# Performance work log

Hardware: AMD Instinct MI355X
Metric: run time of the kernel (lower is better)

## Reference

```python
import jax, jax.numpy as jnp
import numpy as np

B, N, D = 32, 64, 64  # batch, num_points, hidden_dim


def _dense_init(key, fan_in, fan_out):
    kw, kb = jax.random.split(key)
    W = jax.random.normal(kw, (fan_in, fan_out), dtype=jnp.float32) / np.sqrt(fan_in)
    b = jnp.zeros((fan_out,), dtype=jnp.float32)
    return W, b


def setup_inputs() -> dict:
    key = jax.random.key(0)
    ks = jax.random.split(key, 8)
    point_clouds = jax.random.normal(ks[0], (B, N, 3), dtype=jnp.float32)
    Wq, bq = _dense_init(ks[1], 3, D)
    Wk1, bk1 = _dense_init(ks[2], 3, D)
    Wk2, bk2 = _dense_init(ks[3], 3, D)
    Wk3, bk3 = _dense_init(ks[4], 3, D)
    W1, b1 = _dense_init(ks[5], 1, 32)
    W2, b2 = _dense_init(ks[6], 32, 1)
    return {"point_clouds": point_clouds, "Wq": Wq, "bq": bq,
            "Wk1": Wk1, "bk1": bk1, "Wk2": Wk2, "bk2": bk2,
            "Wk3": Wk3, "bk3": bk3, "W1": W1, "b1": b1, "W2": W2, "b2": b2}


def reference(point_clouds, Wq, bq, Wk1, bk1, Wk2, bk2, Wk3, bk3, W1, b1, W2, b2):
    b_sz, n_pts, _ = point_clouds.shape
    hidden = Wq.shape[1]
    scale = jax.lax.rsqrt(jnp.float32(hidden))

    queries = point_clouds @ Wq + bq   # (B,N,D)
    keys_j = point_clouds @ Wk1 + bk1  # (B,N,D)
    keys_k = point_clouds @ Wk2 + bk2
    keys_l = point_clouds @ Wk3 + bk3

    # pairwise key-key attention terms, (B,N,N)
    att_jk = jnp.einsum('bnd,bmd->bnm', keys_j, keys_k) * scale
    att_jl = jnp.einsum('bnd,bmd->bnm', keys_j, keys_l) * scale
    att_kl = jnp.einsum('bnd,bmd->bnm', keys_k, keys_l) * scale

    def process_anchor(carry, xs):
        q_i, p_i = xs  # (B,D), (B,3)
        att_ij = jnp.einsum('bd,bjd->bj', q_i, keys_j) * scale  # (B,N)
        att_ik = jnp.einsum('bd,bkd->bk', q_i, keys_k) * scale
        att_il = jnp.einsum('bd,bld->bl', q_i, keys_l) * scale
        # (B,N,N,N) 6-term additive energy
        energy = (att_ij[:, :, None, None] + att_ik[:, None, :, None]
                  + att_il[:, None, None, :] + att_jk[:, :, :, None]
                  + att_jl[:, :, None, :] + att_kl[:, None, :, :])
        gate = jax.nn.sigmoid(energy)
        disp = point_clouds - p_i[:, None, :]                 # (B,N,3)
        cross_kl = jnp.cross(disp[:, :, None, :], disp[:, None, :, :])  # (B,N,N,3)
        det = jnp.einsum('bjd,bkld->bjkl', disp, cross_kl)     # (B,N,N,N)
        agg = (gate * det * det).sum(axis=(1, 2, 3)) / n_pts ** 3  # (B,)
        return carry, agg

    _, anchor_feats = jax.lax.scan(
        jax.checkpoint(process_anchor), init=None,
        xs=(jnp.swapaxes(queries, 0, 1), jnp.swapaxes(point_clouds, 0, 1)))
    pooled = anchor_feats.mean(axis=0)        # (B,)
    h = jax.nn.gelu(pooled[:, None] @ W1 + b1)  # (B,32), tanh-approx gelu (flax default)
    out = h @ W2 + b2                           # (B,1)
    return out[:, None, :]                      # (B,1,1)
```

## Files before the change

kernel.cpp:

```cpp
#include <hip/hip_runtime.h>
#include <math.h>

#define BB 32
#define NN 64
#define DD 64
constexpr int MAT = BB * NN * NN;
constexpr int DJ_OFF = 6 * MAT;
constexpr int DJ_PER_B = 64 * 32 * 8;
constexpr int POOLED_OFF = DJ_OFF + BB * DJ_PER_B;

typedef float v2f __attribute__((ext_vector_type(2)));

__global__ __launch_bounds__(256) void simplex_phase1(
    const float* __restrict__ pc,
    const float* __restrict__ Wq,  const float* __restrict__ bq,
    const float* __restrict__ Wk1, const float* __restrict__ bk1,
    const float* __restrict__ Wk2, const float* __restrict__ bk2,
    const float* __restrict__ Wk3, const float* __restrict__ bk3,
    float* __restrict__ ws)
{
  const int blk = blockIdx.x;
  const int m   = blk % 7;
  const int b   = blk / 7;
  const int tid = threadIdx.x;

  __shared__ float M[4][4];
  __shared__ float P[NN][3];

  if (m < 6 && tid < 16) {
    int r = tid >> 2, c = tid & 3;
    const float *WA = Wq, *bA = bq, *WB = Wk1, *bB = bk1;
    switch (m) {
      case 0: WA = Wq;  bA = bq;  WB = Wk1; bB = bk1; break;
      case 1: WA = Wq;  bA = bq;  WB = Wk2; bB = bk2; break;
      case 2: WA = Wq;  bA = bq;  WB = Wk3; bB = bk3; break;
      case 3: WA = Wk2; bA = bk2; WB = Wk1; bB = bk1; break;
      case 4: WA = Wk1; bA = bk1; WB = Wk3; bB = bk3; break;
      case 5: WA = Wk2; bA = bk2; WB = Wk3; bB = bk3; break;
    }
    float s = 0.f;
    for (int d = 0; d < DD; ++d) {
      float va = (r < 3) ? WA[r * DD + d] : bA[d];
      float vb = (c < 3) ? WB[c * DD + d] : bB[d];
      s = fmaf(va, vb, s);
    }
    M[r][c] = s;
  }
  if (tid < NN * 3) {
    ((float*)P)[tid] = pc[b * NN * 3 + tid];
  }
  __syncthreads();

  if (m == 6) {
    for (int idx = tid; idx < DJ_PER_B; idx += 256) {
      int word = idx & 7;
      int jp   = (idx >> 3) & 31;
      int i    = idx >> 8;
      float v = 0.f;
      if (word < 6) {
        int axis = word >> 1;
        int j    = jp * 2 + (word & 1);
        v = P[j][axis] - P[i][axis];
      }
      ws[DJ_OFF + b * DJ_PER_B + idx] = v;
    }
    return;
  }

  const float scale2 = -0.125f * 1.4426950408889634f;

  for (int it = 0; it < 16; ++it) {
    int g = tid + 256 * it;
    int r = g >> 6, c = g & 63;
    float ar0 = P[r][0], ar1 = P[r][1], ar2 = P[r][2];
    float ac0 = P[c][0], ac1 = P[c][1], ac2 = P[c][2];
    float t0 = fmaf(M[0][0], ac0, fmaf(M[0][1], ac1, fmaf(M[0][2], ac2, M[0][3])));
    float t1 = fmaf(M[1][0], ac0, fmaf(M[1][1], ac1, fmaf(M[1][2], ac2, M[1][3])));
    float t2 = fmaf(M[2][0], ac0, fmaf(M[2][1], ac1, fmaf(M[2][2], ac2, M[2][3])));
    float t3 = fmaf(M[3][0], ac0, fmaf(M[3][1], ac1, fmaf(M[3][2], ac2, M[3][3])));
    float v = fmaf(ar0, t0, fmaf(ar1, t1, fmaf(ar2, t2, t3))) * scale2;
    if (m == 4) {
      float e = __builtin_amdgcn_exp2f(v);
      ws[4 * MAT + b * 4096 + ((r >> 1) << 7) + (c << 1) + (r & 1)] = e;
    } else if (m == 5) {
      ws[5 * MAT + b * 4096 + g] = __builtin_amdgcn_exp2f(v);
    } else {
      ws[m * MAT + b * 4096 + g] = v;
    }
  }
  if (m == 0 && tid == 0) ws[POOLED_OFF + b] = 0.f;
}

__global__ __launch_bounds__(256, 8) void simplex_main(
    const float* __restrict__ pc,
    const float* __restrict__ ws_in,
    float* __restrict__ pooled)
{
  const int b    = blockIdx.x >> 6;
  const int i    = blockIdx.x & 63;
  const int tid  = threadIdx.x;
  const int lane = tid & 63;
  const int wu   = __builtin_amdgcn_readfirstlane(tid >> 6);

  __shared__ __align__(16) float sE[4096];
  __shared__ float sT[512];
  __shared__ float dX[NN], dY[NN], dZ[NN];
  __shared__ float wsum[4];

  const float* m0  = ws_in + 0 * MAT + (b * 64 + i) * 64;
  const float* m1  = ws_in + 1 * MAT + (b * 64 + i) * 64;
  const float* m2  = ws_in + 2 * MAT + (b * 64 + i) * 64;
  const float* m3  = ws_in + 3 * MAT + b * 4096;
  const float* m4  = ws_in + 4 * MAT + b * 4096;
  const float* m5  = ws_in + 5 * MAT + b * 4096;
  const float* djp = ws_in + DJ_OFF + b * DJ_PER_B + i * 256;

  {
    const float4* src = (const float4*)m4;
    float4* dst = (float4*)sE;
    dst[tid]       = src[tid];
    dst[tid + 256] = src[tid + 256];
    dst[tid + 512] = src[tid + 512];
    dst[tid + 768] = src[tid + 768];
  }
  if (tid < 64) {
    const float pix = pc[(b * 64 + i) * 3 + 0];
    const float piy = pc[(b * 64 + i) * 3 + 1];
    const float piz = pc[(b * 64 + i) * 3 + 2];
    dX[tid] = pc[(b * 64 + tid) * 3 + 0] - pix;
    dY[tid] = pc[(b * 64 + tid) * 3 + 1] - piy;
    dZ[tid] = pc[(b * 64 + tid) * 3 + 2] - piz;
  }
  __syncthreads();

  const float dlx = dX[lane], dly = dY[lane], dlz = dZ[lane];
  const float wl  = __builtin_amdgcn_exp2f(m2[lane]);
  const float aij = m0[lane];
  float* sTw = sT + wu * 128;
  float acc = 0.f;

  for (int kk0 = 2 * wu; kk0 < 64; kk0 += 8) {
    const int kk = __builtin_amdgcn_readfirstlane(kk0);
    v2f cx2[2], cy2[2], cz2[2], mm2[2];
#pragma unroll
    for (int t = 0; t < 2; ++t) {
      const int k = kk + t;
      const float dkx = dX[k], dky = dY[k], dkz = dZ[k];
      const float cx = dky * dlz - dkz * dly;
      const float cy = dkz * dlx - dkx * dlz;
      const float cz = dkx * dly - dky * dlx;
      cx2[t] = (v2f){cx, cx};
      cy2[t] = (v2f){cy, cy};
      cz2[t] = (v2f){cz, cz};
      const float mv = m5[k * 64 + lane] * wl;
      mm2[t] = (v2f){mv, mv};
      const float Tv = __builtin_amdgcn_exp2f(aij + m3[k * 64 + lane] + m1[k]);
      sTw[t * 64 + lane] = Tv;
    }
#pragma unroll 2
    for (int jp = 0; jp < 32; ++jp) {
      const v2f xx = *(const v2f*)(djp + jp * 8 + 0);
      const v2f yy = *(const v2f*)(djp + jp * 8 + 2);
      const v2f zz = *(const v2f*)(djp + jp * 8 + 4);
      const v2f E01 = *(const v2f*)&sE[jp * 128 + lane * 2];
      v2f Tt[2];
      Tt[0] = *(const v2f*)&sTw[2 * jp];
      Tt[1] = *(const v2f*)&sTw[64 + 2 * jp];
#pragma unroll
      for (int t = 0; t < 2; ++t) {
        v2f e01 = E01 * mm2[t];
        v2f x01 = __builtin_elementwise_fma(Tt[t], e01, (v2f){1.f, 1.f});
        v2f det = __builtin_elementwise_fma(xx, cx2[t],
                    __builtin_elementwise_fma(yy, cy2[t], zz * cz2[t]));
        v2f d2  = det * det;
        float den = x01.x * x01.y;
        float rd  = __builtin_amdgcn_rcpf(den);
        float num = fmaf(d2.x, x01.y, d2.y * x01.x);
        acc = fmaf(num, rd, acc);
      }
    }
  }

  for (int s = 32; s; s >>= 1) acc += __shfl_xor(acc, s, 64);
  if (lane == 0) wsum[wu] = acc;
  __syncthreads();
  if (tid == 0) {
    float blocksum = wsum[0] + wsum[1] + wsum[2] + wsum[3];
    atomicAdd(&pooled[b], blocksum * (1.f / 16777216.f));
  }
}

__global__ void simplex_final(
    const float* __restrict__ pooled,
    const float* __restrict__ W1, const float* __restrict__ b1,
    const float* __restrict__ W2, const float* __restrict__ b2,
    float* __restrict__ out)
{
  int t = threadIdx.x;
  if (t < BB) {
    float x = pooled[t];
    float o = b2[0];
    for (int c = 0; c < 32; ++c) {
      float z  = fmaf(x, W1[c], b1[c]);
      float z3 = z * z * z;
      float y  = 0.7978845608028654f * fmaf(0.044715f, z3, z);
      float ay = fabsf(y);
      float e  = __builtin_amdgcn_exp2f(2.8853900817779268f * ay);
      float th = 1.f - 2.f / (e + 1.f);
      th = copysignf(th, y);
      float gl = 0.5f * z * (1.f + th);
      o = fmaf(gl, W2[c], o);
    }
    out[t] = o;
  }
}

extern "C" void kernel_launch(void* const* d_in, const int* in_sizes, int n_in,
                              void* d_out, int out_size, void* d_ws, size_t ws_size,
                              hipStream_t stream) {
  (void)in_sizes; (void)n_in; (void)out_size; (void)ws_size;
  const float* pc  = (const float*)d_in[0];
  const float* Wq  = (const float*)d_in[1];
  const float* bq  = (const float*)d_in[2];
  const float* Wk1 = (const float*)d_in[3];
  const float* bk1 = (const float*)d_in[4];
  const float* Wk2 = (const float*)d_in[5];
  const float* bk2 = (const float*)d_in[6];
  const float* Wk3 = (const float*)d_in[7];
  const float* bk3 = (const float*)d_in[8];
  const float* W1  = (const float*)d_in[9];
  const float* b1  = (const float*)d_in[10];
  const float* W2  = (const float*)d_in[11];
  const float* b2  = (const float*)d_in[12];

  float* ws     = (float*)d_ws;
  float* pooled = ws + POOLED_OFF;
  float* out    = (float*)d_out;

  hipLaunchKernelGGL(simplex_phase1, dim3(BB * 7), dim3(256), 0, stream,
                     pc, Wq, bq, Wk1, bk1, Wk2, bk2, Wk3, bk3, ws);
  hipLaunchKernelGGL(simplex_main, dim3(BB * NN), dim3(256), 0, stream,
                     pc, ws, pooled);
  hipLaunchKernelGGL(simplex_final, dim3(1), dim3(64), 0, stream,
                     pooled, W1, b1, W2, b2, out);
}
```

Before: 190.4 us.

## Move inner energy/det loop to packed fp16 and fuse final MLP via last-block ticket

Switches the innermost loop from fp32 to packed half-precision. The exp factors, the displacements and the cross products are stored as fp16 pairs and accumulated with fdot2, with clamping added to keep values in fp16 range. This is meant to double ALU throughput and halve LDS and global traffic. It also removes the separate final kernel: per-block partial sums go to the workspace and the last block, found with an atomic ticket, computes the GELU MLP. The cost is reduced accuracy from fp16 rounding and clamping, plus a serial tail in the last block.

```diff
diff --git a/kernel.cpp b/kernel.cpp
--- a/kernel.cpp
+++ b/kernel.cpp
@@ -5,11 +5,26 @@
 #define NN 64
 #define DD 64
 constexpr int MAT = BB * NN * NN;
-constexpr int DJ_OFF = 6 * MAT;
-constexpr int DJ_PER_B = 64 * 32 * 8;
-constexpr int POOLED_OFF = DJ_OFF + BB * DJ_PER_B;
-
-typedef float v2f __attribute__((ext_vector_type(2)));
+constexpr int E_OFF    = 5 * MAT;
+constexpr int DJ_OFF   = E_OFF + MAT / 2;
+constexpr int DJ_PER_B = 64 * 32 * 4;
+constexpr int PART_OFF = DJ_OFF + BB * DJ_PER_B;
+constexpr int TICK_OFF = PART_OFF + BB * NN;
+
+typedef _Float16 h2 __attribute__((ext_vector_type(2)));
+
+static __device__ __forceinline__ h2 pkh(float a, float b) {
+  return __builtin_bit_cast(h2, __builtin_amdgcn_cvt_pkrtz(a, b));
+}
+static __device__ __forceinline__ h2 bch(float f) {
+  return __builtin_bit_cast(h2, f);
+}
+static __device__ __forceinline__ h2 rcp2h(h2 x) {
+  h2 r;
+  r.x = static_cast<_Float16>(__builtin_amdgcn_rcph(x.x));
+  r.y = static_cast<_Float16>(__builtin_amdgcn_rcph(x.y));
+  return r;
+}
 
 __global__ __launch_bounds__(256) void simplex_phase1(
     const float* __restrict__ pc,
@@ -53,17 +68,18 @@
 
   if (m == 6) {
     for (int idx = tid; idx < DJ_PER_B; idx += 256) {
-      int word = idx & 7;
-      int jp   = (idx >> 3) & 31;
-      int i    = idx >> 8;
-      float v = 0.f;
-      if (word < 6) {
-        int axis = word >> 1;
-        int j    = jp * 2 + (word & 1);
-        v = P[j][axis] - P[i][axis];
+      int w  = idx & 3;
+      int jp = (idx >> 2) & 31;
+      int i  = idx >> 7;
+      float out = 0.f;
+      if (w < 3) {
+        float v0 = P[2 * jp + 0][w] - P[i][w];
+        float v1 = P[2 * jp + 1][w] - P[i][w];
+        out = __builtin_bit_cast(float, __builtin_amdgcn_cvt_pkrtz(v0, v1));
       }
-      ws[DJ_OFF + b * DJ_PER_B + idx] = v;
-    }
+      ws[DJ_OFF + b * DJ_PER_B + idx] = out;
+    }
+    if (b == 0 && tid == 0) ((int*)(ws + TICK_OFF))[0] = 0;
     return;
   }
 
@@ -80,21 +96,24 @@
     float t3 = fmaf(M[3][0], ac0, fmaf(M[3][1], ac1, fmaf(M[3][2], ac2, M[3][3])));
     float v = fmaf(ar0, t0, fmaf(ar1, t1, fmaf(ar2, t2, t3))) * scale2;
     if (m == 4) {
-      float e = __builtin_amdgcn_exp2f(v);
-      ws[4 * MAT + b * 4096 + ((r >> 1) << 7) + (c << 1) + (r & 1)] = e;
+      float vc = fminf(fmaxf(v, -9.f), 9.f);
+      _Float16 hv = (_Float16)__builtin_amdgcn_exp2f(vc);
+      ((_Float16*)(ws + E_OFF))[b * 4096 + ((r >> 2) << 8) + (c << 2) + (r & 3)] = hv;
     } else if (m == 5) {
-      ws[5 * MAT + b * 4096 + g] = __builtin_amdgcn_exp2f(v);
+      ws[4 * MAT + b * 4096 + g] = __builtin_amdgcn_exp2f(v);
     } else {
       ws[m * MAT + b * 4096 + g] = v;
     }
   }
-  if (m == 0 && tid == 0) ws[POOLED_OFF + b] = 0.f;
 }
 
 __global__ __launch_bounds__(256, 8) void simplex_main(
     const float* __restrict__ pc,
     const float* __restrict__ ws_in,
-    float* __restrict__ pooled)
+    float* __restrict__ ws_rw,
+    const float* __restrict__ W1, const float* __restrict__ b1,
+    const float* __restrict__ W2, const float* __restrict__ b2,
+    float* __restrict__ out)
 {
   const int b    = blockIdx.x >> 6;
   const int i    = blockIdx.x & 63;
@@ -102,26 +121,25 @@
   const int lane = tid & 63;
   const int wu   = __builtin_amdgcn_readfirstlane(tid >> 6);
 
-  __shared__ __align__(16) float sE[4096];
-  __shared__ float sT[512];
+  __shared__ __align__(16) _Float16 sE[4096];
+  __shared__ __align__(16) _Float16 sT[4][128];
   __shared__ float dX[NN], dY[NN], dZ[NN];
   __shared__ float wsum[4];
+  __shared__ int lastFlag;
 
   const float* m0  = ws_in + 0 * MAT + (b * 64 + i) * 64;
   const float* m1  = ws_in + 1 * MAT + (b * 64 + i) * 64;
   const float* m2  = ws_in + 2 * MAT + (b * 64 + i) * 64;
   const float* m3  = ws_in + 3 * MAT + b * 4096;
-  const float* m4  = ws_in + 4 * MAT + b * 4096;
-  const float* m5  = ws_in + 5 * MAT + b * 4096;
-  const float* djp = ws_in + DJ_OFF + b * DJ_PER_B + i * 256;
+  const float* m5R = ws_in + 4 * MAT + b * 4096;
+  const float* Eg  = ws_in + E_OFF + b * 2048;
+  const float* djp = ws_in + DJ_OFF + b * DJ_PER_B + i * 128;
 
   {
-    const float4* src = (const float4*)m4;
+    const float4* src = (const float4*)Eg;
     float4* dst = (float4*)sE;
     dst[tid]       = src[tid];
     dst[tid + 256] = src[tid + 256];
-    dst[tid + 512] = src[tid + 512];
-    dst[tid + 768] = src[tid + 768];
   }
   if (tid < 64) {
     const float pix = pc[(b * 64 + i) * 3 + 0];
@@ -136,12 +154,13 @@
   const float dlx = dX[lane], dly = dY[lane], dlz = dZ[lane];
   const float wl  = __builtin_amdgcn_exp2f(m2[lane]);
   const float aij = m0[lane];
-  float* sTw = sT + wu * 128;
+  _Float16* sTw = &sT[wu][0];
+  const h2 clampE = {(_Float16)8192.f, (_Float16)8192.f};
   float acc = 0.f;
 
-  for (int kk0 = 2 * wu; kk0 < 64; kk0 += 8) {
-    const int kk = __builtin_amdgcn_readfirstlane(kk0);
-    v2f cx2[2], cy2[2], cz2[2], mm2[2];
+  for (int n = 0; n < 8; ++n) {
+    const int kk = __builtin_amdgcn_readfirstlane(n * 8 + 2 * wu);
+    h2 cxh[2], cyh[2], czh[2], mmh[2];
 #pragma unroll
     for (int t = 0; t < 2; ++t) {
       const int k = kk + t;
@@ -149,34 +168,49 @@
       const float cx = dky * dlz - dkz * dly;
       const float cy = dkz * dlx - dkx * dlz;
       const float cz = dkx * dly - dky * dlx;
-      cx2[t] = (v2f){cx, cx};
-      cy2[t] = (v2f){cy, cy};
-      cz2[t] = (v2f){cz, cz};
-      const float mv = m5[k * 64 + lane] * wl;
-      mm2[t] = (v2f){mv, mv};
-      const float Tv = __builtin_amdgcn_exp2f(aij + m3[k * 64 + lane] + m1[k]);
-      sTw[t * 64 + lane] = Tv;
-    }
-#pragma unroll 2
-    for (int jp = 0; jp < 32; ++jp) {
-      const v2f xx = *(const v2f*)(djp + jp * 8 + 0);
-      const v2f yy = *(const v2f*)(djp + jp * 8 + 2);
-      const v2f zz = *(const v2f*)(djp + jp * 8 + 4);
-      const v2f E01 = *(const v2f*)&sE[jp * 128 + lane * 2];
-      v2f Tt[2];
-      Tt[0] = *(const v2f*)&sTw[2 * jp];
-      Tt[1] = *(const v2f*)&sTw[64 + 2 * jp];
+      cxh[t] = pkh(cx, cx);
+      cyh[t] = pkh(cy, cy);
+      czh[t] = pkh(cz, cz);
+      float mv = m5R[k * 64 + lane] * wl;
+      mv = fminf(fmaxf(mv, 0.001953125f), 512.f);
+      mmh[t] = pkh(mv, mv);
+      float logT = aij + m3[k * 64 + lane] + m1[k];
+      logT = fminf(fmaxf(logT, -9.f), 9.f);
+      sTw[t * 64 + lane] = (_Float16)__builtin_amdgcn_exp2f(logT);
+    }
+#pragma unroll 8
+    for (int jg = 0; jg < 16; ++jg) {
+      const float2 Ef = ((const float2*)sE)[jg * 64 + lane];
+      const h2 Ea = bch(Ef.x);
+      const h2 Eb = bch(Ef.y);
+      const float2 T0f = ((const float2*)sTw)[jg];
+      const float2 T1f = ((const float2*)sTw)[16 + jg];
+      const float4 dj0 = *(const float4*)(djp + (2 * jg + 0) * 4);
+      const float4 dj1 = *(const float4*)(djp + (2 * jg + 1) * 4);
+      const h2 xx0 = bch(dj0.x), yy0 = bch(dj0.y), zz0 = bch(dj0.z);
+      const h2 xx1 = bch(dj1.x), yy1 = bch(dj1.y), zz1 = bch(dj1.z);
 #pragma unroll
       for (int t = 0; t < 2; ++t) {
-        v2f e01 = E01 * mm2[t];
-        v2f x01 = __builtin_elementwise_fma(Tt[t], e01, (v2f){1.f, 1.f});
-        v2f det = __builtin_elementwise_fma(xx, cx2[t],
-                    __builtin_elementwise_fma(yy, cy2[t], zz * cz2[t]));
-        v2f d2  = det * det;
-        float den = x01.x * x01.y;
-        float rd  = __builtin_amdgcn_rcpf(den);
-        float num = fmaf(d2.x, x01.y, d2.y * x01.x);
-        acc = fmaf(num, rd, acc);
+        const float2 Tf = t ? T1f : T0f;
+        const h2 Ta = bch(Tf.x), Tb = bch(Tf.y);
+        {
+          h2 e = __builtin_elementwise_min(Ea * mmh[t], clampE);
+          h2 x = __builtin_elementwise_fma(Ta, e,
+                   (h2){(_Float16)1.0f, (_Float16)1.0f});
+          h2 g = rcp2h(x);
+          h2 det = __builtin_elementwise_fma(xx0, cxh[t],
+                     __builtin_elementwise_fma(yy0, cyh[t], zz0 * czh[t]));
+          acc = __builtin_amdgcn_fdot2(g, det * det, acc, false);
+        }
+        {
+          h2 e = __builtin_elementwise_min(Eb * mmh[t], clampE);
+          h2 x = __builtin_elementwise_fma(Tb, e,
+                   (h2){(_Float16)1.0f, (_Float16)1.0f});
+          h2 g = rcp2h(x);
+          h2 det = __builtin_elementwise_fma(xx1, cxh[t],
+                     __builtin_elementwise_fma(yy1, cyh[t], zz1 * czh[t]));
+          acc = __builtin_amdgcn_fdot2(g, det * det, acc, false);
+        }
       }
     }
   }
@@ -186,32 +220,35 @@
   __syncthreads();
   if (tid == 0) {
     float blocksum = wsum[0] + wsum[1] + wsum[2] + wsum[3];
-    atomicAdd(&pooled[b], blocksum * (1.f / 16777216.f));
-  }
-}
-
-__global__ void simplex_final(
-    const float* __restrict__ pooled,
-    const float* __restrict__ W1, const float* __restrict__ b1,
-    const float* __restrict__ W2, const float* __restrict__ b2,
-    float* __restrict__ out)
-{
-  int t = threadIdx.x;
-  if (t < BB) {
-    float x = pooled[t];
-    float o = b2[0];
-    for (int c = 0; c < 32; ++c) {
-      float z  = fmaf(x, W1[c], b1[c]);
-      float z3 = z * z * z;
-      float y  = 0.7978845608028654f * fmaf(0.044715f, z3, z);
-      float ay = fabsf(y);
-      float e  = __builtin_amdgcn_exp2f(2.8853900817779268f * ay);
-      float th = 1.f - 2.f / (e + 1.f);
-      th = copysignf(th, y);
-      float gl = 0.5f * z * (1.f + th);
-      o = fmaf(gl, W2[c], o);
-    }
-    out[t] = o;
+    ws_rw[PART_OFF + blockIdx.x] = blocksum;
+    __threadfence();
+    int old = atomicAdd((int*)(ws_rw + TICK_OFF), 1);
+    lastFlag = (old == (BB * NN - 1));
+  }
+  __syncthreads();
+
+  if (lastFlag) {
+    __threadfence();
+    if (tid < BB) {
+      float s = 0.f;
+      for (int ii = 0; ii < 64; ++ii)
+        s += __hip_atomic_load(ws_rw + PART_OFF + tid * 64 + ii,
+                               __ATOMIC_RELAXED, __HIP_MEMORY_SCOPE_AGENT);
+      float x = s * (1.f / 16777216.f);
+      float o = b2[0];
+      for (int c = 0; c < 32; ++c) {
+        float z  = fmaf(x, W1[c], b1[c]);
+        float z3 = z * z * z;
+        float y  = 0.7978845608028654f * fmaf(0.044715f, z3, z);
+        float ay = fabsf(y);
+        float e  = __builtin_amdgcn_exp2f(2.8853900817779268f * ay);
+        float th = 1.f - 2.f / (e + 1.f);
+        th = copysignf(th, y);
+        float gl = 0.5f * z * (1.f + th);
+        o = fmaf(gl, W2[c], o);
+      }
+      out[tid] = o;
+    }
   }
 }
 
@@ -233,14 +270,11 @@
   const float* W2  = (const float*)d_in[11];
   const float* b2  = (const float*)d_in[12];
 
-  float* ws     = (float*)d_ws;
-  float* pooled = ws + POOLED_OFF;
-  float* out    = (float*)d_out;
+  float* ws  = (float*)d_ws;
+  float* out = (float*)d_out;
 
   hipLaunchKernelGGL(simplex_phase1, dim3(BB * 7), dim3(256), 0, stream,
                      pc, Wq, bq, Wk1, bk1, Wk2, bk2, Wk3, bk3, ws);
   hipLaunchKernelGGL(simplex_main, dim3(BB * NN), dim3(256), 0, stream,
-                     pc, ws, pooled);
-  hipLaunchKernelGGL(simplex_final, dim3(1), dim3(64), 0, stream,
-                     pooled, W1, b1, W2, b2, out);
-}
+                     pc, ws, ws, W1, b1, W2, b2, out);
+}
```

Measured after the change: 206.2 us. +8.3%, slower.
